# Optimization experiments

Measured on AMD Instinct MI355X. Metric: run time of the kernel, lower is better.

Reference implementation:

```python
import jax, jax.numpy as jnp
import numpy as np

N_NODES = 100000
N_EDGES = 6400000
N_FEAT = 128
HIDDEN = 16
OUT = 2
N_GRAPHS = 64


def setup_inputs() -> dict:
    key = jax.random.key(0)
    ks = jax.random.split(key, 8)
    x = jax.random.normal(ks[0], (N_NODES, N_FEAT), dtype=jnp.float32)
    edge_index = jax.random.randint(ks[1], (2, N_EDGES), 0, N_NODES, dtype=jnp.int64)
    batch_idx = jnp.sort(jax.random.randint(ks[2], (N_NODES,), 0, N_GRAPHS, dtype=jnp.int64))
    # GCNConv params (Glorot-ish scale)
    W1 = jax.random.normal(ks[3], (N_FEAT, HIDDEN), dtype=jnp.float32) / np.sqrt(N_FEAT)
    b1 = jnp.zeros((HIDDEN,), dtype=jnp.float32)
    prelu_a = jnp.full((1,), 0.25, dtype=jnp.float32)  # torch.nn.PReLU default
    W2 = jax.random.normal(ks[4], (HIDDEN, OUT), dtype=jnp.float32) / np.sqrt(HIDDEN)
    b2 = jnp.zeros((OUT,), dtype=jnp.float32)
    return {"x": x, "W1": W1, "b1": b1, "prelu_a": prelu_a, "W2": W2, "b2": b2,
            "edge_index": edge_index, "batch_idx": batch_idx}


def _gcn_conv(h, W, b, src, dst, norm, n_nodes):
    h = h @ W                                  # [N, d_out]
    msg = h[src] * norm[:, None]               # gather + normalize, [E', d_out]
    agg = jax.ops.segment_sum(msg, dst, num_segments=n_nodes)  # scatter-add
    return agg + b


def reference(x, W1, b1, prelu_a, W2, b2, edge_index, batch_idx):
    n_nodes = x.shape[0]
    # GCNConv default: add self-loops, symmetric normalization D^-1/2 A D^-1/2
    loops = jnp.arange(n_nodes, dtype=edge_index.dtype)
    src = jnp.concatenate([edge_index[0], loops])
    dst = jnp.concatenate([edge_index[1], loops])
    deg = jax.ops.segment_sum(jnp.ones_like(dst, dtype=x.dtype), dst, num_segments=n_nodes)
    dinv = jnp.where(deg > 0, jax.lax.rsqrt(deg), 0.0)
    norm = dinv[src] * dinv[dst]               # [E']

    h = _gcn_conv(x, W1, b1, src, dst, norm, n_nodes)
    h = jnp.where(h >= 0, h, prelu_a * h)      # PReLU (single shared slope)
    h = _gcn_conv(h, W2, b2, src, dst, norm, n_nodes)

    # global mean pool over graphs
    sums = jax.ops.segment_sum(h, batch_idx, num_segments=N_GRAPHS)
    cnts = jax.ops.segment_sum(jnp.ones((n_nodes,), dtype=h.dtype), batch_idx, num_segments=N_GRAPHS)
    return sums / jnp.maximum(cnts, 1.0)[:, None]
```

## Files before the change

kernel.cpp:

```cpp
#include <hip/hip_runtime.h>

#define NFEAT 128
#define HID 16
#define NOUT 2
#define NGRAPH 64

#define BN 196
#define NBUCK 512
#define NCB 512
#define CH 12500
#define EPT 13
#define CAP 13824
#define PSTRIDE 192
#define WST 132
#define ACST 9

#define S20F 1048576.0f
#define S20I 9.5367431640625e-7f
#define S18F 262144.0f
#define S18I 3.814697265625e-6f
#define SPF  32768.0f
#define SPI  3.0517578125e-5f
#define OFF23 0x800000
#define OFF22 0x400000

typedef unsigned short ushortv8 __attribute__((ext_vector_type(8)));
typedef float fvec4 __attribute__((ext_vector_type(4)));

__device__ __forceinline__ int chunk_id(int bid) { return ((bid & 7) << 6) | (bid >> 3); }

__device__ __forceinline__ unsigned short f2bf(float f) {
    unsigned u = __float_as_uint(f);
    return (unsigned short)((u + 0x7FFFu + ((u >> 16) & 1u)) >> 16);
}

__device__ __forceinline__ float bf2f(unsigned short b) {
    return __uint_as_float(((unsigned)b) << 16);
}

__device__ __forceinline__ unsigned bucket_of(int d) { return (unsigned)d / (unsigned)BN; }

__global__ __launch_bounds__(1024) void k_scatter(const int* __restrict__ src, const int* __restrict__ dst,
                                                  int* __restrict__ cursor,
                                                  unsigned int* __restrict__ bpk, int E) {
    __shared__ unsigned int stage[CH + 44];
    __shared__ int hist4[4 * NBUCK];
    __shared__ int scan[512];
    __shared__ int excl[NBUCK + 1];
    __shared__ int cur[NBUCK];
    int t = threadIdx.x;
    int cid = chunk_id(blockIdx.x);
    int start = cid * CH;
    int end = min(E, start + CH);
    for (int i = t; i < 4 * NBUCK; i += 1024) hist4[i] = 0;
    __syncthreads();

    unsigned int w[EPT];
    int kb[EPT];
    int rep = (t & 3) * NBUCK;
    #pragma unroll
    for (int i = 0; i < EPT; i++) {
        int e = start + i * 1024 + t;
        kb[i] = -1;
        if (e < end) {
            int s = __builtin_nontemporal_load(src + e);
            int d = __builtin_nontemporal_load(dst + e);
            unsigned b = bucket_of(d);
            int dl = d - (int)(b * BN);
            kb[i] = (int)b;
            w[i] = ((unsigned)dl << 17) | (unsigned)s;
            atomicAdd(&hist4[rep + (int)b], 1);
        }
    }
    __syncthreads();

    int hc = 0, gb = 0;
    if (t < NBUCK) {
        hc = hist4[t] + hist4[NBUCK + t] + hist4[2 * NBUCK + t] + hist4[3 * NBUCK + t];
        if (hc > 0) gb = atomicAdd(&cursor[t], hc);
    }
    if (t < 512) scan[t] = (t < NBUCK) ? hc : 0;
    __syncthreads();
    for (int off = 1; off < 512; off <<= 1) {
        int a = 0;
        if (t < 512 && t >= off) a = scan[t - off];
        __syncthreads();
        if (t < 512 && t >= off) scan[t] += a;
        __syncthreads();
    }
    if (t < NBUCK) {
        int ex = scan[t] - hc;
        excl[t] = ex;
        cur[t] = ex;
        hist4[t] = gb;
    }
    if (t == 0) excl[NBUCK] = end - start;
    __syncthreads();

    #pragma unroll
    for (int i = 0; i < EPT; i++) {
        if (kb[i] >= 0) {
            int r = atomicAdd(&cur[kb[i]], 1);
            stage[r] = w[i];
        }
    }
    __syncthreads();

    int wave = t >> 6, lane = t & 63;
    for (int b = wave; b < NBUCK; b += 16) {
        int s0 = excl[b], s1 = excl[b + 1];
        int run = s1 - s0;
        if (run <= 0) continue;
        int gbase = hist4[b];
        int avail = CAP - gbase;
        int lim = min(run, max(avail, 0));
        for (int j = lane; j < lim; j += 64)
            bpk[(size_t)b * CAP + gbase + j] = stage[s0 + j];
    }
}

__global__ __launch_bounds__(1024) void k_deg(const unsigned int* __restrict__ bpk, const int* __restrict__ cursor,
                                              float* __restrict__ dinv, int* __restrict__ deg, int N) {
    __shared__ int h[BN];
    int t = threadIdx.x;
    int k = blockIdx.x;
    if (t < BN) h[t] = 0;
    __syncthreads();
    int bstart = k * CAP;
    int bend = bstart + cursor[k];
    for (int e = bstart + t; e < bend; e += 1024)
        atomicAdd(&h[__builtin_nontemporal_load(bpk + e) >> 17], 1);
    __syncthreads();
    if (t < BN) {
        int gn = k * BN + t;
        if (gn < N) {
            deg[gn] = h[t];
            dinv[gn] = rsqrtf(1.0f + (float)h[t]);
        }
    }
}

__global__ __launch_bounds__(256) void k_xw1(const float* __restrict__ x, const float* __restrict__ W1,
                                             const float* __restrict__ dinv,
                                             unsigned short* __restrict__ h1b, int N) {
    __shared__ float sWT[HID * WST];
    __shared__ float sx[16 * 132];
    int t = threadIdx.x;
    for (int i = t; i < HID * NFEAT; i += 256) {
        int h = i >> 7, kk = i & 127;
        sWT[h * WST + kk] = W1[kk * HID + h];
    }
    int local = t >> 4;
    int h     = t & 15;
    int n = blockIdx.x * 16 + local;
    if (n < N) {
        const fvec4* xr = (const fvec4*)(x + (size_t)n * NFEAT);
        fvec4 a = __builtin_nontemporal_load(xr + h * 2);
        fvec4 b = __builtin_nontemporal_load(xr + h * 2 + 1);
        float* sp = sx + local * 132 + h * 8;
        ((fvec4*)sp)[0] = a;
        ((fvec4*)sp)[1] = b;
    }
    __syncthreads();
    if (n >= N) return;
    const fvec4* xr4 = (const fvec4*)(sx + local * 132);
    const fvec4* wr4 = (const fvec4*)(sWT + h * WST);
    float acc = 0.0f;
    #pragma unroll
    for (int k4 = 0; k4 < 32; k4++) {
        fvec4 a = xr4[k4];
        fvec4 b = wr4[k4];
        acc += a.x * b.x + a.y * b.y + a.z * b.z + a.w * b.w;
    }
    h1b[(size_t)n * HID + h] = f2bf(acc * dinv[n]);
}

__global__ __launch_bounds__(1024) void k_bg1(const unsigned int* __restrict__ bpk, const int* __restrict__ cursor,
                                              const unsigned short* __restrict__ h1b, const float* __restrict__ dinv,
                                              const int* __restrict__ deg,
                                              const float* __restrict__ b1, const float* __restrict__ prelu_a,
                                              const float* __restrict__ W2,
                                              float* __restrict__ t2s, int N) {
    __shared__ unsigned long long acc[BN * ACST];
    int t = threadIdx.x;
    int k = blockIdx.x;
    for (int i = t; i < BN * ACST; i += 1024) acc[i] = 0ull;
    __syncthreads();
    int bstart = k * CAP;
    int bend = bstart + cursor[k];
    int q = t & 1;
    const uint4* h4 = (const uint4*)h1b;

    int e = bstart + (t >> 1);
    unsigned int w = (e < bend) ? __builtin_nontemporal_load(bpk + e) : 0u;
    while (e < bend) {
        int e2 = e + 512;
        unsigned int wn = (e2 < bend) ? __builtin_nontemporal_load(bpk + e2) : 0u;
        int d = (int)(w >> 17);
        int s = (int)(w & 0x1FFFFu);
        uint4 u = h4[(size_t)s * 2 + q];
        unsigned long long* ap = acc + d * ACST + q * 4;
        #pragma unroll
        for (int jj = 0; jj < 4; jj++) {
            unsigned uu = (&u.x)[jj];
            float flo = __uint_as_float((uu << 16) + 0x0A000000u);
            float fhi = __uint_as_float((uu & 0xFFFF0000u) + 0x0A000000u);
            unsigned lo = (unsigned)(__float2int_rn(flo) + OFF23);
            unsigned hi = (unsigned)(__float2int_rn(fhi) + OFF23);
            atomicAdd(&ap[jj], ((unsigned long long)hi << 32) | (unsigned long long)lo);
        }
        w = wn;
        e = e2;
    }
    __syncthreads();

    if (t < BN * 2) {
        int n = t >> 1;
        int qq = t & 1;
        int gn = k * BN + n;
        if (gn < N) {
            float di = dinv[gn];
            int dg = deg[gn];
            long long bias = (long long)dg << 23;
            float a = prelu_a[0];
            const ushortv8* h8 = (const ushortv8*)h1b;
            ushortv8 sv = h8[(size_t)gn * 2 + qq];
            float o0 = 0.0f, o1 = 0.0f;
            #pragma unroll
            for (int jj = 0; jj < 4; jj++) {
                unsigned long long av = acc[n * ACST + qq * 4 + jj];
                float f0 = (float)((long long)(unsigned)av - bias) * S20I;
                float f1 = (float)((long long)(av >> 32) - bias) * S20I;
                int fa = qq * 8 + 2 * jj;
                float tv = di * (f0 + bf2f(sv[2 * jj])) + b1[fa];
                tv = (tv >= 0.0f) ? tv : a * tv;
                o0 += tv * W2[fa * 2 + 0];
                o1 += tv * W2[fa * 2 + 1];
                int fb = fa + 1;
                float tw = di * (f1 + bf2f(sv[2 * jj + 1])) + b1[fb];
                tw = (tw >= 0.0f) ? tw : a * tw;
                o0 += tw * W2[fb * 2 + 0];
                o1 += tw * W2[fb * 2 + 1];
            }
            o0 += __shfl_xor(o0, 1);
            o1 += __shfl_xor(o1, 1);
            if (qq == 0)
                *(float2*)(t2s + (size_t)gn * 2) = make_float2(di * o0, di * o1);
        }
    }
}

__global__ __launch_bounds__(1024) void k_bg2(const unsigned int* __restrict__ bpk, const int* __restrict__ cursor,
                                              const float* __restrict__ t2s, const float* __restrict__ dinv,
                                              const int* __restrict__ deg, const int* __restrict__ batch,
                                              int* __restrict__ bins, int N) {
    __shared__ unsigned long long acc2[BN];
    __shared__ int pg[PSTRIDE];
    int t = threadIdx.x;
    int k = blockIdx.x;
    if (t < BN) acc2[t] = 0ull;
    if (t < PSTRIDE) pg[t] = 0;
    __syncthreads();
    int bstart = k * CAP;
    int bend = bstart + cursor[k];

    int e = bstart + t;
    unsigned int w = (e < bend) ? __builtin_nontemporal_load(bpk + e) : 0u;
    while (e < bend) {
        int e2 = e + 1024;
        unsigned int wn = (e2 < bend) ? __builtin_nontemporal_load(bpk + e2) : 0u;
        int d = (int)(w >> 17);
        int s = (int)(w & 0x1FFFFu);
        float2 v = *(const float2*)(t2s + (size_t)s * 2);
        unsigned lo = (unsigned)(__float2int_rn(v.x * S18F) + OFF22);
        unsigned hi = (unsigned)(__float2int_rn(v.y * S18F) + OFF22);
        atomicAdd(&acc2[d], ((unsigned long long)hi << 32) | (unsigned long long)lo);
        w = wn;
        e = e2;
    }
    __syncthreads();
    if (t < BN) {
        int gn = k * BN + t;
        if (gn < N) {
            float dd = dinv[gn];
            int dg = deg[gn];
            long long bias = (long long)dg << 22;
            unsigned long long av = acc2[t];
            float2 self = *(const float2*)(t2s + (size_t)gn * 2);
            float v0 = (float)((long long)(unsigned)av - bias) * S18I + self.x;
            float v1 = (float)((long long)(av >> 32) - bias) * S18I + self.y;
            int g = batch[gn];
            atomicAdd(&pg[g * 2 + 0], __float2int_rn(dd * v0 * SPF));
            atomicAdd(&pg[g * 2 + 1], __float2int_rn(dd * v1 * SPF));
            atomicAdd(&pg[128 + g], 1);
        }
    }
    __syncthreads();
    if (t < PSTRIDE && pg[t] != 0) atomicAdd(&bins[t], pg[t]);
}

__global__ __launch_bounds__(128) void k_final(const int* __restrict__ bins,
                                               const float* __restrict__ b2, float* __restrict__ out) {
    int t = threadIdx.x;
    if (t < NGRAPH * NOUT) {
        int g = t >> 1, c = t & 1;
        float cnt = (float)bins[128 + g];
        float val = (float)bins[t] * SPI;
        out[t] = (val + cnt * b2[c]) / fmaxf(cnt, 1.0f);
    }
}

extern "C" void kernel_launch(void* const* d_in, const int* in_sizes, int n_in,
                              void* d_out, int out_size, void* d_ws, size_t ws_size,
                              hipStream_t stream) {
    const float* x       = (const float*)d_in[0];
    const float* W1      = (const float*)d_in[1];
    const float* b1      = (const float*)d_in[2];
    const float* prelu_a = (const float*)d_in[3];
    const float* W2      = (const float*)d_in[4];
    const float* b2      = (const float*)d_in[5];
    const int*   ei      = (const int*)d_in[6];
    const int*   batch   = (const int*)d_in[7];

    const int N = in_sizes[7];
    const int E = in_sizes[6] / 2;
    const int* src = ei;
    const int* dst = ei + E;

    float* ws     = (float*)d_ws;
    float* dinv   = ws;
    int*   deg    = (int*)(dinv + 100352);
    unsigned short* h1b = (unsigned short*)(deg + 100352);
    float* t2s    = (float*)((int*)h1b + 802816);
    int*   cursor = (int*)(t2s + 200064);
    int*   bins   = cursor + 512;
    unsigned int* bpk = (unsigned int*)(bins + 256);

    float* out = (float*)d_out;

    hipMemsetAsync(cursor, 0, (512 + 256) * sizeof(int), stream);
    k_scatter<<<NCB, 1024, 0, stream>>>(src, dst, cursor, bpk, E);
    k_deg<<<NBUCK, 1024, 0, stream>>>(bpk, cursor, dinv, deg, N);
    k_xw1<<<(N + 15) / 16, 256, 0, stream>>>(x, W1, dinv, h1b, N);
    k_bg1<<<NBUCK, 1024, 0, stream>>>(bpk, cursor, h1b, dinv, deg, b1, prelu_a, W2, t2s, N);
    k_bg2<<<NBUCK, 1024, 0, stream>>>(bpk, cursor, t2s, dinv, deg, batch, bins, N);
    k_final<<<1, 128, 0, stream>>>(bins, b2, out);
}
```

Baseline: 264.2 us.

## Fuse degree and XW1 kernels, split LDS accumulators and unroll edge loops

Merges the degree histogram kernel with the X·W1 projection so each bucket block computes its own nodes' dinv in shared memory and then projects their features, removing one launch and the global dinv reload. The bg1 and bg2 edge loops now process two edges per iteration and send atomics to two LDS accumulator copies, which are summed at the end. This is meant to cut LDS atomic contention and raise memory-level parallelism. In exchange it uses more shared memory and registers, and the fused kernel's projection runs on only 512 blocks instead of many small ones.

```diff
diff --git a/kernel.cpp b/kernel.cpp
--- a/kernel.cpp
+++ b/kernel.cpp
@@ -119,98 +119,120 @@
     }
 }
 
-__global__ __launch_bounds__(1024) void k_deg(const unsigned int* __restrict__ bpk, const int* __restrict__ cursor,
-                                              float* __restrict__ dinv, int* __restrict__ deg, int N) {
-    __shared__ int h[BN];
+__global__ __launch_bounds__(1024) void k_degw1(const unsigned int* __restrict__ bpk, const int* __restrict__ cursor,
+                                                const float* __restrict__ x, const float* __restrict__ W1,
+                                                int* __restrict__ deg, float* __restrict__ dinv,
+                                                unsigned short* __restrict__ h1b, int N) {
+    __shared__ int hdeg[BN];
+    __shared__ float sdinv[BN];
+    __shared__ float sWT[HID * WST];
+    __shared__ float sx[64 * 132];
     int t = threadIdx.x;
     int k = blockIdx.x;
-    if (t < BN) h[t] = 0;
+    if (t < BN) hdeg[t] = 0;
+    for (int i = t; i < HID * NFEAT; i += 1024) {
+        int h = i >> 7, kk = i & 127;
+        sWT[h * WST + kk] = W1[kk * HID + h];
+    }
     __syncthreads();
     int bstart = k * CAP;
     int bend = bstart + cursor[k];
     for (int e = bstart + t; e < bend; e += 1024)
-        atomicAdd(&h[__builtin_nontemporal_load(bpk + e) >> 17], 1);
+        atomicAdd(&hdeg[__builtin_nontemporal_load(bpk + e) >> 17], 1);
     __syncthreads();
     if (t < BN) {
         int gn = k * BN + t;
-        if (gn < N) {
-            deg[gn] = h[t];
-            dinv[gn] = rsqrtf(1.0f + (float)h[t]);
-        }
-    }
-}
-
-__global__ __launch_bounds__(256) void k_xw1(const float* __restrict__ x, const float* __restrict__ W1,
-                                             const float* __restrict__ dinv,
-                                             unsigned short* __restrict__ h1b, int N) {
-    __shared__ float sWT[HID * WST];
-    __shared__ float sx[16 * 132];
-    int t = threadIdx.x;
-    for (int i = t; i < HID * NFEAT; i += 256) {
-        int h = i >> 7, kk = i & 127;
-        sWT[h * WST + kk] = W1[kk * HID + h];
-    }
+        float di = rsqrtf(1.0f + (float)hdeg[t]);
+        sdinv[t] = di;
+        if (gn < N) { deg[gn] = hdeg[t]; dinv[gn] = di; }
+    }
+    __syncthreads();
+
     int local = t >> 4;
     int h     = t & 15;
-    int n = blockIdx.x * 16 + local;
-    if (n < N) {
-        const fvec4* xr = (const fvec4*)(x + (size_t)n * NFEAT);
-        fvec4 a = __builtin_nontemporal_load(xr + h * 2);
-        fvec4 b = __builtin_nontemporal_load(xr + h * 2 + 1);
-        float* sp = sx + local * 132 + h * 8;
-        ((fvec4*)sp)[0] = a;
-        ((fvec4*)sp)[1] = b;
-    }
-    __syncthreads();
-    if (n >= N) return;
-    const fvec4* xr4 = (const fvec4*)(sx + local * 132);
-    const fvec4* wr4 = (const fvec4*)(sWT + h * WST);
-    float acc = 0.0f;
-    #pragma unroll
-    for (int k4 = 0; k4 < 32; k4++) {
-        fvec4 a = xr4[k4];
-        fvec4 b = wr4[k4];
-        acc += a.x * b.x + a.y * b.y + a.z * b.z + a.w * b.w;
-    }
-    h1b[(size_t)n * HID + h] = f2bf(acc * dinv[n]);
-}
-
-__global__ __launch_bounds__(1024) void k_bg1(const unsigned int* __restrict__ bpk, const int* __restrict__ cursor,
-                                              const unsigned short* __restrict__ h1b, const float* __restrict__ dinv,
-                                              const int* __restrict__ deg,
-                                              const float* __restrict__ b1, const float* __restrict__ prelu_a,
-                                              const float* __restrict__ W2,
-                                              float* __restrict__ t2s, int N) {
-    __shared__ unsigned long long acc[BN * ACST];
+    for (int nb = 0; nb < 4; nb++) {
+        int ln = nb * 64 + local;
+        int gn = k * BN + ln;
+        bool valid = (ln < BN) && (gn < N);
+        if (valid) {
+            const fvec4* xr = (const fvec4*)(x + (size_t)gn * NFEAT);
+            fvec4 a = __builtin_nontemporal_load(xr + h * 2);
+            fvec4 b = __builtin_nontemporal_load(xr + h * 2 + 1);
+            float* sp = sx + local * 132 + h * 8;
+            ((fvec4*)sp)[0] = a;
+            ((fvec4*)sp)[1] = b;
+        }
+        __syncthreads();
+        if (valid) {
+            const fvec4* xr4 = (const fvec4*)(sx + local * 132);
+            const fvec4* wr4 = (const fvec4*)(sWT + h * WST);
+            float acc = 0.0f;
+            #pragma unroll
+            for (int k4 = 0; k4 < 32; k4++) {
+                fvec4 a = xr4[k4];
+                fvec4 b = wr4[k4];
+                acc += a.x * b.x + a.y * b.y + a.z * b.z + a.w * b.w;
+            }
+            h1b[(size_t)gn * HID + h] = f2bf(acc * sdinv[ln]);
+        }
+        __syncthreads();
+    }
+}
+
+__global__ __launch_bounds__(1024, 8) void k_bg1(const unsigned int* __restrict__ bpk, const int* __restrict__ cursor,
+                                                 const unsigned short* __restrict__ h1b, const float* __restrict__ dinv,
+                                                 const int* __restrict__ deg,
+                                                 const float* __restrict__ b1, const float* __restrict__ prelu_a,
+                                                 const float* __restrict__ W2,
+                                                 float* __restrict__ t2s, int N) {
+    __shared__ unsigned long long acc[2][BN * ACST];
     int t = threadIdx.x;
     int k = blockIdx.x;
-    for (int i = t; i < BN * ACST; i += 1024) acc[i] = 0ull;
+    for (int i = t; i < 2 * BN * ACST; i += 1024) ((unsigned long long*)acc)[i] = 0ull;
     __syncthreads();
     int bstart = k * CAP;
     int bend = bstart + cursor[k];
     int q = t & 1;
+    int cp = (t >> 1) & 1;
+    unsigned long long* myacc = acc[cp];
     const uint4* h4 = (const uint4*)h1b;
 
     int e = bstart + (t >> 1);
-    unsigned int w = (e < bend) ? __builtin_nontemporal_load(bpk + e) : 0u;
+    unsigned int w0 = (e < bend) ? __builtin_nontemporal_load(bpk + e) : 0u;
+    unsigned int w1 = (e + 512 < bend) ? __builtin_nontemporal_load(bpk + e + 512) : 0u;
     while (e < bend) {
-        int e2 = e + 512;
-        unsigned int wn = (e2 < bend) ? __builtin_nontemporal_load(bpk + e2) : 0u;
-        int d = (int)(w >> 17);
-        int s = (int)(w & 0x1FFFFu);
-        uint4 u = h4[(size_t)s * 2 + q];
-        unsigned long long* ap = acc + d * ACST + q * 4;
+        int eN = e + 1024;
+        unsigned int w0n = (eN < bend) ? __builtin_nontemporal_load(bpk + eN) : 0u;
+        unsigned int w1n = (eN + 512 < bend) ? __builtin_nontemporal_load(bpk + eN + 512) : 0u;
+        bool hasB = (e + 512 < bend);
+        int dA = (int)(w0 >> 17), sA = (int)(w0 & 0x1FFFFu);
+        int dB = (int)(w1 >> 17), sB = (int)(w1 & 0x1FFFFu);
+        uint4 uA = h4[(size_t)sA * 2 + q];
+        uint4 uB;
+        if (hasB) uB = h4[(size_t)sB * 2 + q];
+        unsigned long long* apA = myacc + dA * ACST + q * 4;
         #pragma unroll
         for (int jj = 0; jj < 4; jj++) {
-            unsigned uu = (&u.x)[jj];
+            unsigned uu = (&uA.x)[jj];
             float flo = __uint_as_float((uu << 16) + 0x0A000000u);
             float fhi = __uint_as_float((uu & 0xFFFF0000u) + 0x0A000000u);
             unsigned lo = (unsigned)(__float2int_rn(flo) + OFF23);
             unsigned hi = (unsigned)(__float2int_rn(fhi) + OFF23);
-            atomicAdd(&ap[jj], ((unsigned long long)hi << 32) | (unsigned long long)lo);
-        }
-        w = wn;
-        e = e2;
+            atomicAdd(&apA[jj], ((unsigned long long)hi << 32) | (unsigned long long)lo);
+        }
+        if (hasB) {
+            unsigned long long* apB = myacc + dB * ACST + q * 4;
+            #pragma unroll
+            for (int jj = 0; jj < 4; jj++) {
+                unsigned uu = (&uB.x)[jj];
+                float flo = __uint_as_float((uu << 16) + 0x0A000000u);
+                float fhi = __uint_as_float((uu & 0xFFFF0000u) + 0x0A000000u);
+                unsigned lo = (unsigned)(__float2int_rn(flo) + OFF23);
+                unsigned hi = (unsigned)(__float2int_rn(fhi) + OFF23);
+                atomicAdd(&apB[jj], ((unsigned long long)hi << 32) | (unsigned long long)lo);
+            }
+        }
+        w0 = w0n; w1 = w1n; e = eN;
     }
     __syncthreads();
 
@@ -228,9 +250,12 @@
             float o0 = 0.0f, o1 = 0.0f;
             #pragma unroll
             for (int jj = 0; jj < 4; jj++) {
-                unsigned long long av = acc[n * ACST + qq * 4 + jj];
-                float f0 = (float)((long long)(unsigned)av - bias) * S20I;
-                float f1 = (float)((long long)(av >> 32) - bias) * S20I;
+                unsigned long long a0 = acc[0][n * ACST + qq * 4 + jj];
+                unsigned long long a1 = acc[1][n * ACST + qq * 4 + jj];
+                long long losum = (long long)(unsigned)a0 + (long long)(unsigned)a1;
+                long long hisum = (long long)(a0 >> 32) + (long long)(a1 >> 32);
+                float f0 = (float)(losum - bias) * S20I;
+                float f1 = (float)(hisum - bias) * S20I;
                 int fa = qq * 8 + 2 * jj;
                 float tv = di * (f0 + bf2f(sv[2 * jj])) + b1[fa];
                 tv = (tv >= 0.0f) ? tv : a * tv;
@@ -250,33 +275,46 @@
     }
 }
 
-__global__ __launch_bounds__(1024) void k_bg2(const unsigned int* __restrict__ bpk, const int* __restrict__ cursor,
-                                              const float* __restrict__ t2s, const float* __restrict__ dinv,
-                                              const int* __restrict__ deg, const int* __restrict__ batch,
-                                              int* __restrict__ bins, int N) {
-    __shared__ unsigned long long acc2[BN];
+__global__ __launch_bounds__(1024, 8) void k_bg2(const unsigned int* __restrict__ bpk, const int* __restrict__ cursor,
+                                                 const float* __restrict__ t2s, const float* __restrict__ dinv,
+                                                 const int* __restrict__ deg, const int* __restrict__ batch,
+                                                 int* __restrict__ bins, int N) {
+    __shared__ unsigned long long acc2[2][BN];
     __shared__ int pg[PSTRIDE];
     int t = threadIdx.x;
     int k = blockIdx.x;
-    if (t < BN) acc2[t] = 0ull;
+    for (int i = t; i < 2 * BN; i += 1024) ((unsigned long long*)acc2)[i] = 0ull;
     if (t < PSTRIDE) pg[t] = 0;
     __syncthreads();
     int bstart = k * CAP;
     int bend = bstart + cursor[k];
+    int cp = t & 1;
+    unsigned long long* myacc = acc2[cp];
 
     int e = bstart + t;
-    unsigned int w = (e < bend) ? __builtin_nontemporal_load(bpk + e) : 0u;
+    unsigned int w0 = (e < bend) ? __builtin_nontemporal_load(bpk + e) : 0u;
+    unsigned int w1 = (e + 1024 < bend) ? __builtin_nontemporal_load(bpk + e + 1024) : 0u;
     while (e < bend) {
-        int e2 = e + 1024;
-        unsigned int wn = (e2 < bend) ? __builtin_nontemporal_load(bpk + e2) : 0u;
-        int d = (int)(w >> 17);
-        int s = (int)(w & 0x1FFFFu);
-        float2 v = *(const float2*)(t2s + (size_t)s * 2);
-        unsigned lo = (unsigned)(__float2int_rn(v.x * S18F) + OFF22);
-        unsigned hi = (unsigned)(__float2int_rn(v.y * S18F) + OFF22);
-        atomicAdd(&acc2[d], ((unsigned long long)hi << 32) | (unsigned long long)lo);
-        w = wn;
-        e = e2;
+        int eN = e + 2048;
+        unsigned int w0n = (eN < bend) ? __builtin_nontemporal_load(bpk + eN) : 0u;
+        unsigned int w1n = (eN + 1024 < bend) ? __builtin_nontemporal_load(bpk + eN + 1024) : 0u;
+        bool hasB = (e + 1024 < bend);
+        int dA = (int)(w0 >> 17), sA = (int)(w0 & 0x1FFFFu);
+        int dB = (int)(w1 >> 17), sB = (int)(w1 & 0x1FFFFu);
+        float2 vA = *(const float2*)(t2s + (size_t)sA * 2);
+        float2 vB;
+        if (hasB) vB = *(const float2*)(t2s + (size_t)sB * 2);
+        {
+            unsigned lo = (unsigned)(__float2int_rn(vA.x * S18F) + OFF22);
+            unsigned hi = (unsigned)(__float2int_rn(vA.y * S18F) + OFF22);
+            atomicAdd(&myacc[dA], ((unsigned long long)hi << 32) | (unsigned long long)lo);
+        }
+        if (hasB) {
+            unsigned lo = (unsigned)(__float2int_rn(vB.x * S18F) + OFF22);
+            unsigned hi = (unsigned)(__float2int_rn(vB.y * S18F) + OFF22);
+            atomicAdd(&myacc[dB], ((unsigned long long)hi << 32) | (unsigned long long)lo);
+        }
+        w0 = w0n; w1 = w1n; e = eN;
     }
     __syncthreads();
     if (t < BN) {
@@ -285,10 +323,13 @@
             float dd = dinv[gn];
             int dg = deg[gn];
             long long bias = (long long)dg << 22;
-            unsigned long long av = acc2[t];
+            unsigned long long a0 = acc2[0][t];
+            unsigned long long a1 = acc2[1][t];
+            long long losum = (long long)(unsigned)a0 + (long long)(unsigned)a1;
+            long long hisum = (long long)(a0 >> 32) + (long long)(a1 >> 32);
             float2 self = *(const float2*)(t2s + (size_t)gn * 2);
-            float v0 = (float)((long long)(unsigned)av - bias) * S18I + self.x;
-            float v1 = (float)((long long)(av >> 32) - bias) * S18I + self.y;
+            float v0 = (float)(losum - bias) * S18I + self.x;
+            float v1 = (float)(hisum - bias) * S18I + self.y;
             int g = batch[gn];
             atomicAdd(&pg[g * 2 + 0], __float2int_rn(dd * v0 * SPF));
             atomicAdd(&pg[g * 2 + 1], __float2int_rn(dd * v1 * SPF));
@@ -340,8 +381,7 @@
 
     hipMemsetAsync(cursor, 0, (512 + 256) * sizeof(int), stream);
     k_scatter<<<NCB, 1024, 0, stream>>>(src, dst, cursor, bpk, E);
-    k_deg<<<NBUCK, 1024, 0, stream>>>(bpk, cursor, dinv, deg, N);
-    k_xw1<<<(N + 15) / 16, 256, 0, stream>>>(x, W1, dinv, h1b, N);
+    k_degw1<<<NBUCK, 1024, 0, stream>>>(bpk, cursor, x, W1, deg, dinv, h1b, N);
     k_bg1<<<NBUCK, 1024, 0, stream>>>(bpk, cursor, h1b, dinv, deg, b1, prelu_a, W2, t2s, N);
     k_bg2<<<NBUCK, 1024, 0, stream>>>(bpk, cursor, t2s, dinv, deg, batch, bins, N);
     k_final<<<1, 128, 0, stream>>>(bins, b2, out);
```

Result: faster. 254.6 us (-3.6%).
